# Optimization experiments

Measured on AMD Instinct MI355X. Metric: run time of the kernel, lower is better.

Reference implementation:

```python
import jax, jax.numpy as jnp
import numpy as np

BN_EPSILON = 1e-05


def hard_sigmoid(x):
    return jnp.clip((x + 1.0) / 2.0, 0.0, 1.0)


def setup_inputs() -> dict:
    key = jax.random.key(0)
    kx, kw, kb = jax.random.split(key, 3)
    # NHWC activations
    x = jax.random.normal(kx, (64, 112, 112, 64), dtype=jnp.float32)
    # HWIO kernel initialized ~ truncated_normal(stddev=0.2), then Bernoulli-binarized
    # to +/-1 once at graph-construction time (set_input_shape), so we sample here.
    k_init = 0.2 * jax.random.normal(kw, (3, 3, 64, 64), dtype=jnp.float32)
    kernels = 2.0 * jax.random.bernoulli(kb, hard_sigmoid(k_init)).astype(jnp.float32) - 1.0
    # tf.contrib.layers.batch_norm defaults: center=True (beta), scale=False (no gamma)
    beta = jnp.zeros((64,), dtype=jnp.float32)
    return {"x": x, "kernels": kernels, "beta": beta}


def reference(x, kernels, beta):
    # Training-mode batch norm: per-batch moments over (N, H, W)
    mean = jnp.mean(x, axis=(0, 1, 2))
    var = jnp.var(x, axis=(0, 1, 2))
    x_bn = (x - mean) * jax.lax.rsqrt(var + BN_EPSILON) + beta
    # NOTE: original code computes conv(sign(x_bn), k) but immediately overwrites it
    # with conv(x_bn, k); the effective forward uses the batch-normed (non-signed)
    # activations with the binarized (+/-1) kernels.
    a = jax.lax.conv_general_dilated(
        x_bn, kernels,
        window_strides=(1, 1),
        padding="SAME",
        dimension_numbers=("NHWC", "HWIO", "NHWC"),
    )
    return a
```

## Files before the change

kernel.cpp:

```cpp
#include <hip/hip_runtime.h>

typedef __attribute__((ext_vector_type(8))) short bf16x8;
typedef __attribute__((ext_vector_type(8))) unsigned short u16x8;
typedef __attribute__((ext_vector_type(4))) unsigned short u16x4;
typedef __attribute__((ext_vector_type(4))) float f32x4;

#define HW      112
#define CH      64
#define PIX_IMG (HW*HW)
#define N4TOT   (64*112*112*64/4)
#define NPIX_F  802816.0f

#define WS_HV_BYTE  1280
#define WS_W_BYTE   4096
#define WS_XBF_BYTE (4u<<20)

__device__ __forceinline__ unsigned short f2bf(float f) {
  unsigned u = __float_as_uint(f);
  u += 0x7FFFu + ((u >> 16) & 1u);
  return (unsigned short)(u >> 16);
}

__global__ void zero_ws(float* __restrict__ ws) {
  ws[threadIdx.x] = 0.0f;
}

template <bool WRITE_BF>
__global__ __launch_bounds__(256) void stats_kernel(const float* __restrict__ x,
                                                    float* __restrict__ ws,
                                                    unsigned short* __restrict__ xbf) {
  __shared__ float red[128];
  const int tid = threadIdx.x;
  if (tid < 128) red[tid] = 0.0f;
  __syncthreads();

  const f32x4* __restrict__ x4 = (const f32x4*)x;
  f32x4 s = {0.f, 0.f, 0.f, 0.f};
  f32x4 q = {0.f, 0.f, 0.f, 0.f};
  const int stride = gridDim.x * 256;
  #pragma unroll 4
  for (int i = blockIdx.x * 256 + tid; i < N4TOT; i += stride) {
    f32x4 v = __builtin_nontemporal_load(&x4[i]);
    s += v;
    q += v * v;
    if (WRITE_BF) {
      u16x4 o = {f2bf(v[0]), f2bf(v[1]), f2bf(v[2]), f2bf(v[3])};
      *(u16x4*)(xbf + 4 * i) = o;
    }
  }
  #pragma unroll
  for (int m = 16; m <= 32; m <<= 1) {
    #pragma unroll
    for (int j = 0; j < 4; ++j) {
      s[j] += __shfl_xor(s[j], m);
      q[j] += __shfl_xor(q[j], m);
    }
  }
  if ((tid & 63) < 16) {
    const int c0 = (tid & 15) * 4;
    #pragma unroll
    for (int j = 0; j < 4; ++j) {
      atomicAdd(&red[c0 + j], s[j]);
      atomicAdd(&red[64 + c0 + j], q[j]);
    }
  }
  __syncthreads();
  if (tid < 128) atomicAdd(&ws[tid], red[tid]);
}

__global__ __launch_bounds__(256) void finalize_kernel(const float* __restrict__ beta,
                                                       const float* __restrict__ k,
                                                       float* __restrict__ ws) {
  __shared__ float sb[64];
  __shared__ float part[256];
  const int tid = threadIdx.x;
  if (tid < 64) {
    float mean = ws[tid] * (1.0f / NPIX_F);
    float var  = fmaxf(ws[64 + tid] * (1.0f / NPIX_F) - mean * mean, 0.0f);
    float sc = rsqrtf(var + 1e-5f);
    float b  = beta[tid] - mean * sc;
    ws[128 + tid] = sc;
    ws[192 + tid] = b;
    ((unsigned short*)((char*)ws + WS_HV_BYTE))[tid] = f2bf(-b / sc);
    sb[tid] = b;
  }
  __syncthreads();
  const int co = tid & 63, pt = tid >> 6;
  float a = 0.f;
  #pragma unroll 8
  for (int t = pt; t < 576; t += 4)
    a = fmaf(sb[t & 63], k[t * 64 + co], a);
  part[tid] = a;
  __syncthreads();
  if (tid < 64)
    ws[256 + tid] = part[tid] + part[64 + tid] + part[128 + tid] + part[192 + tid];
}

__global__ __launch_bounds__(256) void prep_w(const float* __restrict__ k,
                                              const float* __restrict__ ws,
                                              unsigned short* __restrict__ wsw) {
  const int oidx = blockIdx.x * 256 + threadIdx.x;
  const int j  = oidx & 7;
  const int co = (oidx >> 3) & 63;
  const int qd = (oidx >> 9) & 3;
  const int t2 = oidx >> 11;
  const int tap = t2 % 9;
  const int h   = t2 / 9;
  const int ci  = h * 32 + qd * 8 + j;
  wsw[oidx] = f2bf(k[(tap * 64 + ci) * 64 + co] * ws[128 + ci]);
}

template <bool USE_BF>
__global__ __launch_bounds__(448, 4) void conv_kernel(const float* __restrict__ x,
                                                      const unsigned short* __restrict__ xbf,
                                                      const unsigned short* __restrict__ wsw,
                                                      const float* __restrict__ ws,
                                                      float* __restrict__ out) {
  __shared__ unsigned short Xs[4 * 6 * 114 * 8];
  __shared__ unsigned short Wd[2304 * 8];
  const int tid = threadIdx.x;
  int bid = (int)blockIdx.x;
  bid = (bid & 7) * 224 + (bid >> 3);
  const int n  = bid / 28;
  const int h0 = (bid % 28) * 4;

  const int lane = tid & 63;
  const int wv   = tid >> 6;
  const int qd   = lane >> 4;
  const int cc   = lane & 15;
  const int wvb  = wv * 16;

  const unsigned short* hv = (const unsigned short*)((const char*)ws + WS_HV_BYTE);

  f32x4 acc[4][4];
  {
    const float* bo = ws + 256;
    #pragma unroll
    for (int mt = 0; mt < 4; ++mt) {
      const f32x4 bv = *(const f32x4*)(bo + mt * 16 + qd * 4);
      #pragma unroll
      for (int r = 0; r < 4; ++r) acc[r][mt] = bv;
    }
  }

  for (int half = 0; half < 2; ++half) {
    {
      u16x8 hv8[4];
      #pragma unroll
      for (int o = 0; o < 4; ++o) hv8[o] = *(const u16x8*)(hv + half * 32 + o * 8);
      auto stage = [&](int c) {
        const int o  = c & 3;
        const int pi = c >> 2;
        const int p  = pi % 114;
        const int r  = pi / 114;
        const int w  = p - 1;
        const int g  = h0 + r - 1;
        u16x8 v;
        if ((unsigned)w < 112u && (unsigned)g < 112u) {
          const int base = ((n * 112 + g) * 112 + w) * 64 + half * 32 + o * 8;
          if (USE_BF) {
            v = *(const u16x8*)(xbf + base);
          } else {
            const float* sp = x + base;
            const f32x4 a = *(const f32x4*)sp;
            const f32x4 b = *(const f32x4*)(sp + 4);
            v = (u16x8){f2bf(a[0]), f2bf(a[1]), f2bf(a[2]), f2bf(a[3]),
                        f2bf(b[0]), f2bf(b[1]), f2bf(b[2]), f2bf(b[3])};
          }
        } else {
          v = hv8[o];
        }
        *(u16x8*)(&Xs[o * 5472 + pi * 8]) = v;
      };
      #pragma unroll
      for (int kk = 0; kk < 6; ++kk) stage(kk * 448 + tid);
      if (tid < 48) stage(2688 + tid);
    }
    {
      const unsigned short* wh = wsw + half * 18432;
      auto wstage = [&](int t) {
        *(u16x8*)(&Wd[t * 8]) = *(const u16x8*)(wh + t * 8);
      };
      #pragma unroll
      for (int kk = 0; kk < 5; ++kk) wstage(kk * 448 + tid);
      if (tid < 64) wstage(2240 + tid);
    }
    __syncthreads();

    #pragma unroll
    for (int dw = 0; dw < 3; ++dw) {
      bf16x8 xb[4];
      #pragma unroll
      for (int rr = 0; rr < 4; ++rr)
        xb[rr] = *(const bf16x8*)(&Xs[qd * 5472 + (rr * 114 + wvb + dw + cc) * 8]);
      #pragma unroll
      for (int dh = 0; dh < 3; ++dh) {
        if (dh)
          xb[(dh + 3) & 3] =
              *(const bf16x8*)(&Xs[qd * 5472 + ((dh + 3) * 114 + wvb + dw + cc) * 8]);
        #pragma unroll
        for (int mt = 0; mt < 4; ++mt) {
          const bf16x8 wa = *(const bf16x8*)(
              &Wd[(((dh * 3 + dw) * 4 + qd) * 64 + mt * 16 + cc) * 8]);
          #pragma unroll
          for (int r = 0; r < 4; ++r)
            acc[r][mt] = __builtin_amdgcn_mfma_f32_16x16x32_bf16(wa, xb[(dh + r) & 3],
                                                                 acc[r][mt], 0, 0, 0);
        }
      }
    }
    if (half == 0) __syncthreads();
  }

  #pragma unroll
  for (int r = 0; r < 4; ++r) {
    const int pix = n * PIX_IMG + (h0 + r) * 112 + wvb + cc;
    float* op = out + pix * 64 + qd * 4;
    #pragma unroll
    for (int mt = 0; mt < 4; ++mt)
      *(f32x4*)(op + mt * 16) = acc[r][mt];
  }
}

extern "C" void kernel_launch(void* const* d_in, const int* in_sizes, int n_in,
                              void* d_out, int out_size, void* d_ws, size_t ws_size,
                              hipStream_t stream) {
  const float* x    = (const float*)d_in[0];
  const float* kern = (const float*)d_in[1];
  const float* beta = (const float*)d_in[2];
  float* out = (float*)d_out;
  float* ws  = (float*)d_ws;
  unsigned short* wsw = (unsigned short*)((char*)d_ws + WS_W_BYTE);
  unsigned short* xbf = (unsigned short*)((char*)d_ws + WS_XBF_BYTE);

  const bool use_bf = ws_size >= (size_t)WS_XBF_BYTE + 102760448ull;

  zero_ws<<<1, 128, 0, stream>>>(ws);
  if (use_bf) stats_kernel<true ><<<2048, 256, 0, stream>>>(x, ws, xbf);
  else        stats_kernel<false><<<2048, 256, 0, stream>>>(x, ws, xbf);
  finalize_kernel<<<1, 256, 0, stream>>>(beta, kern, ws);
  prep_w<<<144, 256, 0, stream>>>(kern, ws, wsw);
  if (use_bf) conv_kernel<true ><<<64 * 28, 448, 0, stream>>>(x, xbf, wsw, ws, out);
  else        conv_kernel<false><<<64 * 28, 448, 0, stream>>>(x, xbf, wsw, ws, out);
}
```

Baseline: 493.3 us.

## Give each wave a private input tile, prefetch second channel half, fuse finalize/prep

The conv kernel now loads all weights for both channel halves into shared memory once. Each wave gets its own 6x18 halo tile, so the block-wide barriers between halves go away. Global loads for the second channel half go into registers before the first half's MFMA work and are written to the wave's tile afterwards, overlapping memory with compute. Finalize and weight-prep are merged into one launch, and the block-index swizzle is dropped. The trade is more LDS per block (launch bounds cut from 4 to 2 blocks per CU, so lower occupancy), more register pressure from the prefetch buffer, and redundant halo loads across neighbouring waves.

```diff
diff --git a/kernel.cpp b/kernel.cpp
--- a/kernel.cpp
+++ b/kernel.cpp
@@ -68,9 +68,11 @@
   if (tid < 128) atomicAdd(&ws[tid], red[tid]);
 }
 
-__global__ __launch_bounds__(256) void finalize_kernel(const float* __restrict__ beta,
-                                                       const float* __restrict__ k,
-                                                       float* __restrict__ ws) {
+__global__ __launch_bounds__(256) void finalize_prep(const float* __restrict__ beta,
+                                                     const float* __restrict__ k,
+                                                     float* __restrict__ ws,
+                                                     unsigned short* __restrict__ wsw) {
+  __shared__ float scl[64];
   __shared__ float sb[64];
   __shared__ float part[256];
   const int tid = threadIdx.x;
@@ -79,48 +81,48 @@
     float var  = fmaxf(ws[64 + tid] * (1.0f / NPIX_F) - mean * mean, 0.0f);
     float sc = rsqrtf(var + 1e-5f);
     float b  = beta[tid] - mean * sc;
-    ws[128 + tid] = sc;
-    ws[192 + tid] = b;
-    ((unsigned short*)((char*)ws + WS_HV_BYTE))[tid] = f2bf(-b / sc);
-    sb[tid] = b;
-  }
-  __syncthreads();
-  const int co = tid & 63, pt = tid >> 6;
-  float a = 0.f;
-  #pragma unroll 8
-  for (int t = pt; t < 576; t += 4)
-    a = fmaf(sb[t & 63], k[t * 64 + co], a);
-  part[tid] = a;
-  __syncthreads();
-  if (tid < 64)
-    ws[256 + tid] = part[tid] + part[64 + tid] + part[128 + tid] + part[192 + tid];
-}
-
-__global__ __launch_bounds__(256) void prep_w(const float* __restrict__ k,
-                                              const float* __restrict__ ws,
-                                              unsigned short* __restrict__ wsw) {
-  const int oidx = blockIdx.x * 256 + threadIdx.x;
-  const int j  = oidx & 7;
-  const int co = (oidx >> 3) & 63;
-  const int qd = (oidx >> 9) & 3;
-  const int t2 = oidx >> 11;
-  const int tap = t2 % 9;
-  const int h   = t2 / 9;
-  const int ci  = h * 32 + qd * 8 + j;
-  wsw[oidx] = f2bf(k[(tap * 64 + ci) * 64 + co] * ws[128 + ci]);
+    scl[tid] = sc;
+    sb[tid]  = b;
+    if (blockIdx.x == 0)
+      ((unsigned short*)((char*)ws + WS_HV_BYTE))[tid] = f2bf(-b / sc);
+  }
+  __syncthreads();
+
+  {
+    const int oidx = blockIdx.x * 256 + tid;
+    const int j  = oidx & 7;
+    const int co = (oidx >> 3) & 63;
+    const int qd = (oidx >> 9) & 3;
+    const int t2 = oidx >> 11;
+    const int tap = t2 % 9;
+    const int h   = t2 / 9;
+    const int ci  = h * 32 + qd * 8 + j;
+    wsw[oidx] = f2bf(k[(tap * 64 + ci) * 64 + co] * scl[ci]);
+  }
+
+  if (blockIdx.x == 0) {
+    const int co = tid & 63, pt = tid >> 6;
+    float a = 0.f;
+    #pragma unroll 8
+    for (int t = pt; t < 576; t += 4)
+      a = fmaf(sb[t & 63], k[t * 64 + co], a);
+    part[tid] = a;
+    __syncthreads();
+    if (tid < 64)
+      ws[256 + tid] = part[tid] + part[64 + tid] + part[128 + tid] + part[192 + tid];
+  }
 }
 
 template <bool USE_BF>
-__global__ __launch_bounds__(448, 4) void conv_kernel(const float* __restrict__ x,
+__global__ __launch_bounds__(448, 2) void conv_kernel(const float* __restrict__ x,
                                                       const unsigned short* __restrict__ xbf,
                                                       const unsigned short* __restrict__ wsw,
                                                       const float* __restrict__ ws,
                                                       float* __restrict__ out) {
-  __shared__ unsigned short Xs[4 * 6 * 114 * 8];
-  __shared__ unsigned short Wd[2304 * 8];
+  __shared__ unsigned short Xs[7 * 3456];
+  __shared__ unsigned short Wd[36864];
   const int tid = threadIdx.x;
-  int bid = (int)blockIdx.x;
-  bid = (bid & 7) * 224 + (bid >> 3);
+  const int bid = (int)blockIdx.x;
   const int n  = bid / 28;
   const int h0 = (bid % 28) * 4;
 
@@ -131,6 +133,7 @@
   const int wvb  = wv * 16;
 
   const unsigned short* hv = (const unsigned short*)((const char*)ws + WS_HV_BYTE);
+  unsigned short* Xw = &Xs[wv * 3456];
 
   f32x4 acc[4][4];
   {
@@ -143,21 +146,25 @@
     }
   }
 
-  for (int half = 0; half < 2; ++half) {
-    {
-      u16x8 hv8[4];
-      #pragma unroll
-      for (int o = 0; o < 4; ++o) hv8[o] = *(const u16x8*)(hv + half * 32 + o * 8);
-      auto stage = [&](int c) {
-        const int o  = c & 3;
-        const int pi = c >> 2;
-        const int p  = pi % 114;
-        const int r  = pi / 114;
-        const int w  = p - 1;
-        const int g  = h0 + r - 1;
+  for (int t = tid; t < 4608; t += 448)
+    *(u16x8*)(&Wd[t * 8]) = *(const u16x8*)(wsw + t * 8);
+  __syncthreads();
+
+
+  {
+    u16x8 hv8[4];
+    #pragma unroll
+    for (int o = 0; o < 4; ++o) hv8[o] = *(const u16x8*)(hv + o * 8);
+    #pragma unroll
+    for (int kk = 0; kk < 7; ++kk) {
+      const int e = kk * 64 + lane;
+      if (kk < 6 || lane < 48) {
+        const int o = e & 3, r2 = e >> 2;
+        const int px = r2 % 18, row = r2 / 18;
+        const int w = wvb + px - 1, g = h0 + row - 1;
         u16x8 v;
         if ((unsigned)w < 112u && (unsigned)g < 112u) {
-          const int base = ((n * 112 + g) * 112 + w) * 64 + half * 32 + o * 8;
+          const int base = ((n * 112 + g) * 112 + w) * 64 + o * 8;
           if (USE_BF) {
             v = *(const u16x8*)(xbf + base);
           } else {
@@ -170,38 +177,44 @@
         } else {
           v = hv8[o];
         }
-        *(u16x8*)(&Xs[o * 5472 + pi * 8]) = v;
-      };
-      #pragma unroll
-      for (int kk = 0; kk < 6; ++kk) stage(kk * 448 + tid);
-      if (tid < 48) stage(2688 + tid);
-    }
-    {
-      const unsigned short* wh = wsw + half * 18432;
-      auto wstage = [&](int t) {
-        *(u16x8*)(&Wd[t * 8]) = *(const u16x8*)(wh + t * 8);
-      };
-      #pragma unroll
-      for (int kk = 0; kk < 5; ++kk) wstage(kk * 448 + tid);
-      if (tid < 64) wstage(2240 + tid);
-    }
-    __syncthreads();
-
+        *(u16x8*)(&Xw[o * 864 + r2 * 8]) = v;
+      }
+    }
+  }
+
+  u16x8 pf[7];
+  if (USE_BF) {
+    #pragma unroll
+    for (int kk = 0; kk < 7; ++kk) {
+      const int e = kk * 64 + lane;
+      if (kk < 6 || lane < 48) {
+        const int o = e & 3, r2 = e >> 2;
+        const int px = r2 % 18, row = r2 / 18;
+        const int w = wvb + px - 1, g = h0 + row - 1;
+        if ((unsigned)w < 112u && (unsigned)g < 112u)
+          pf[kk] = *(const u16x8*)(xbf + ((n * 112 + g) * 112 + w) * 64 + 32 + o * 8);
+      }
+    }
+    __builtin_amdgcn_sched_barrier(0);
+  }
+
+  auto compute = [&](int half) {
+    const int wb = half * 18432;
     #pragma unroll
     for (int dw = 0; dw < 3; ++dw) {
       bf16x8 xb[4];
       #pragma unroll
       for (int rr = 0; rr < 4; ++rr)
-        xb[rr] = *(const bf16x8*)(&Xs[qd * 5472 + (rr * 114 + wvb + dw + cc) * 8]);
+        xb[rr] = *(const bf16x8*)(&Xw[qd * 864 + (rr * 18 + dw + cc) * 8]);
       #pragma unroll
       for (int dh = 0; dh < 3; ++dh) {
         if (dh)
           xb[(dh + 3) & 3] =
-              *(const bf16x8*)(&Xs[qd * 5472 + ((dh + 3) * 114 + wvb + dw + cc) * 8]);
+              *(const bf16x8*)(&Xw[qd * 864 + ((dh + 3) * 18 + dw + cc) * 8]);
         #pragma unroll
         for (int mt = 0; mt < 4; ++mt) {
           const bf16x8 wa = *(const bf16x8*)(
-              &Wd[(((dh * 3 + dw) * 4 + qd) * 64 + mt * 16 + cc) * 8]);
+              &Wd[wb + (((dh * 3 + dw) * 4 + qd) * 64 + mt * 16 + cc) * 8]);
           #pragma unroll
           for (int r = 0; r < 4; ++r)
             acc[r][mt] = __builtin_amdgcn_mfma_f32_16x16x32_bf16(wa, xb[(dh + r) & 3],
@@ -209,8 +222,42 @@
         }
       }
     }
-    if (half == 0) __syncthreads();
-  }
+  };
+
+  compute(0);
+
+  {
+    u16x8 hv8[4];
+    #pragma unroll
+    for (int o = 0; o < 4; ++o) hv8[o] = *(const u16x8*)(hv + 32 + o * 8);
+    #pragma unroll
+    for (int kk = 0; kk < 7; ++kk) {
+      const int e = kk * 64 + lane;
+      if (kk < 6 || lane < 48) {
+        const int o = e & 3, r2 = e >> 2;
+        const int px = r2 % 18, row = r2 / 18;
+        const int w = wvb + px - 1, g = h0 + row - 1;
+        const bool ok = (unsigned)w < 112u && (unsigned)g < 112u;
+        u16x8 v;
+        if (USE_BF) {
+          v = ok ? pf[kk] : hv8[o];
+        } else {
+          if (ok) {
+            const float* sp = x + ((n * 112 + g) * 112 + w) * 64 + 32 + o * 8;
+            const f32x4 a = *(const f32x4*)sp;
+            const f32x4 b = *(const f32x4*)(sp + 4);
+            v = (u16x8){f2bf(a[0]), f2bf(a[1]), f2bf(a[2]), f2bf(a[3]),
+                        f2bf(b[0]), f2bf(b[1]), f2bf(b[2]), f2bf(b[3])};
+          } else {
+            v = hv8[o];
+          }
+        }
+        *(u16x8*)(&Xw[o * 864 + r2 * 8]) = v;
+      }
+    }
+  }
+
+  compute(1);
 
   #pragma unroll
   for (int r = 0; r < 4; ++r) {
@@ -238,8 +285,7 @@
   zero_ws<<<1, 128, 0, stream>>>(ws);
   if (use_bf) stats_kernel<true ><<<2048, 256, 0, stream>>>(x, ws, xbf);
   else        stats_kernel<false><<<2048, 256, 0, stream>>>(x, ws, xbf);
-  finalize_kernel<<<1, 256, 0, stream>>>(beta, kern, ws);
-  prep_w<<<144, 256, 0, stream>>>(kern, ws, wsw);
+  finalize_prep<<<144, 256, 0, stream>>>(beta, kern, ws, wsw);
   if (use_bf) conv_kernel<true ><<<64 * 28, 448, 0, stream>>>(x, xbf, wsw, ws, out);
   else        conv_kernel<false><<<64 * 28, 448, 0, stream>>>(x, xbf, wsw, ws, out);
 }
```

Measured after the change: 517.6 us. +4.9%, slower.

## Use per-wave LDS input tiles, split row staging, fuse finalize with weight prep

Applied to the files above, without the earlier changes.

The conv kernel now stages a private 6-row by 18-pixel input strip per wave instead of one shared tile for the whole block. The first four rows are computed before the last two are loaded, so waves no longer wait on each other for input data and LDS use drops. The blockIdx swizzle is removed. The separate finalize and prep_w kernels are merged into one 144-block launch, removing a launch and a dependency, at the cost of every block recomputing the BN scale. The per-wave halo pixels are loaded redundantly, and dropping the swizzle may change L2 locality.

```diff
diff --git a/kernel.cpp b/kernel.cpp
--- a/kernel.cpp
+++ b/kernel.cpp
@@ -68,9 +68,11 @@
   if (tid < 128) atomicAdd(&ws[tid], red[tid]);
 }
 
-__global__ __launch_bounds__(256) void finalize_kernel(const float* __restrict__ beta,
-                                                       const float* __restrict__ k,
-                                                       float* __restrict__ ws) {
+__global__ __launch_bounds__(256) void finalize_prep(const float* __restrict__ beta,
+                                                     const float* __restrict__ k,
+                                                     float* __restrict__ ws,
+                                                     unsigned short* __restrict__ wsw) {
+  __shared__ float scl[64];
   __shared__ float sb[64];
   __shared__ float part[256];
   const int tid = threadIdx.x;
@@ -79,35 +81,36 @@
     float var  = fmaxf(ws[64 + tid] * (1.0f / NPIX_F) - mean * mean, 0.0f);
     float sc = rsqrtf(var + 1e-5f);
     float b  = beta[tid] - mean * sc;
-    ws[128 + tid] = sc;
-    ws[192 + tid] = b;
-    ((unsigned short*)((char*)ws + WS_HV_BYTE))[tid] = f2bf(-b / sc);
-    sb[tid] = b;
-  }
-  __syncthreads();
-  const int co = tid & 63, pt = tid >> 6;
-  float a = 0.f;
-  #pragma unroll 8
-  for (int t = pt; t < 576; t += 4)
-    a = fmaf(sb[t & 63], k[t * 64 + co], a);
-  part[tid] = a;
-  __syncthreads();
-  if (tid < 64)
-    ws[256 + tid] = part[tid] + part[64 + tid] + part[128 + tid] + part[192 + tid];
-}
-
-__global__ __launch_bounds__(256) void prep_w(const float* __restrict__ k,
-                                              const float* __restrict__ ws,
-                                              unsigned short* __restrict__ wsw) {
-  const int oidx = blockIdx.x * 256 + threadIdx.x;
-  const int j  = oidx & 7;
-  const int co = (oidx >> 3) & 63;
-  const int qd = (oidx >> 9) & 3;
-  const int t2 = oidx >> 11;
-  const int tap = t2 % 9;
-  const int h   = t2 / 9;
-  const int ci  = h * 32 + qd * 8 + j;
-  wsw[oidx] = f2bf(k[(tap * 64 + ci) * 64 + co] * ws[128 + ci]);
+    scl[tid] = sc;
+    sb[tid]  = b;
+    if (blockIdx.x == 0)
+      ((unsigned short*)((char*)ws + WS_HV_BYTE))[tid] = f2bf(-b / sc);
+  }
+  __syncthreads();
+
+  {
+    const int oidx = blockIdx.x * 256 + tid;
+    const int j  = oidx & 7;
+    const int co = (oidx >> 3) & 63;
+    const int qd = (oidx >> 9) & 3;
+    const int t2 = oidx >> 11;
+    const int tap = t2 % 9;
+    const int h   = t2 / 9;
+    const int ci  = h * 32 + qd * 8 + j;
+    wsw[oidx] = f2bf(k[(tap * 64 + ci) * 64 + co] * scl[ci]);
+  }
+
+  if (blockIdx.x == 0) {
+    const int co = tid & 63, pt = tid >> 6;
+    float a = 0.f;
+    #pragma unroll 8
+    for (int t = pt; t < 576; t += 4)
+      a = fmaf(sb[t & 63], k[t * 64 + co], a);
+    part[tid] = a;
+    __syncthreads();
+    if (tid < 64)
+      ws[256 + tid] = part[tid] + part[64 + tid] + part[128 + tid] + part[192 + tid];
+  }
 }
 
 template <bool USE_BF>
@@ -116,11 +119,10 @@
                                                       const unsigned short* __restrict__ wsw,
                                                       const float* __restrict__ ws,
                                                       float* __restrict__ out) {
-  __shared__ unsigned short Xs[4 * 6 * 114 * 8];
-  __shared__ unsigned short Wd[2304 * 8];
+  __shared__ unsigned short Xs[7 * 2304];
+  __shared__ unsigned short Wd[18432];
   const int tid = threadIdx.x;
-  int bid = (int)blockIdx.x;
-  bid = (bid & 7) * 224 + (bid >> 3);
+  const int bid = (int)blockIdx.x;
   const int n  = bid / 28;
   const int h0 = (bid % 28) * 4;
 
@@ -131,6 +133,7 @@
   const int wvb  = wv * 16;
 
   const unsigned short* hv = (const unsigned short*)((const char*)ws + WS_HV_BYTE);
+  unsigned short* Xw = &Xs[wv * 2304];
 
   f32x4 acc[4][4];
   {
@@ -143,74 +146,112 @@
     }
   }
 
-  for (int half = 0; half < 2; ++half) {
-    {
-      u16x8 hv8[4];
-      #pragma unroll
-      for (int o = 0; o < 4; ++o) hv8[o] = *(const u16x8*)(hv + half * 32 + o * 8);
-      auto stage = [&](int c) {
-        const int o  = c & 3;
-        const int pi = c >> 2;
-        const int p  = pi % 114;
-        const int r  = pi / 114;
-        const int w  = p - 1;
-        const int g  = h0 + r - 1;
-        u16x8 v;
-        if ((unsigned)w < 112u && (unsigned)g < 112u) {
-          const int base = ((n * 112 + g) * 112 + w) * 64 + half * 32 + o * 8;
-          if (USE_BF) {
-            v = *(const u16x8*)(xbf + base);
-          } else {
-            const float* sp = x + base;
-            const f32x4 a = *(const f32x4*)sp;
-            const f32x4 b = *(const f32x4*)(sp + 4);
-            v = (u16x8){f2bf(a[0]), f2bf(a[1]), f2bf(a[2]), f2bf(a[3]),
-                        f2bf(b[0]), f2bf(b[1]), f2bf(b[2]), f2bf(b[3])};
-          }
-        } else {
-          v = hv8[o];
-        }
-        *(u16x8*)(&Xs[o * 5472 + pi * 8]) = v;
-      };
-      #pragma unroll
-      for (int kk = 0; kk < 6; ++kk) stage(kk * 448 + tid);
-      if (tid < 48) stage(2688 + tid);
-    }
-    {
-      const unsigned short* wh = wsw + half * 18432;
-      auto wstage = [&](int t) {
-        *(u16x8*)(&Wd[t * 8]) = *(const u16x8*)(wh + t * 8);
-      };
-      #pragma unroll
-      for (int kk = 0; kk < 5; ++kk) wstage(kk * 448 + tid);
-      if (tid < 64) wstage(2240 + tid);
-    }
-    __syncthreads();
-
+  auto ld = [&](int g, int w, int q, int half, const u16x8 hv8[4]) -> u16x8 {
+    if ((unsigned)w < 112u && (unsigned)g < 112u) {
+      const int base = ((n * 112 + g) * 112 + w) * 64 + half * 32 + q * 8;
+      if (USE_BF) {
+        return *(const u16x8*)(xbf + base);
+      } else {
+        const float* sp = x + base;
+        const f32x4 a = *(const f32x4*)sp;
+        const f32x4 b = *(const f32x4*)(sp + 4);
+        return (u16x8){f2bf(a[0]), f2bf(a[1]), f2bf(a[2]), f2bf(a[3]),
+                       f2bf(b[0]), f2bf(b[1]), f2bf(b[2]), f2bf(b[3])};
+      }
+    }
+    return hv8[q];
+  };
+
+  auto stageA = [&](int half) {
+    u16x8 hv8[4];
+    #pragma unroll
+    for (int o = 0; o < 4; ++o) hv8[o] = *(const u16x8*)(hv + half * 32 + o * 8);
+    #pragma unroll
+    for (int kk = 0; kk < 5; ++kk) {
+      const int c = kk * 64 + lane;
+      if (kk < 4 || lane < 32) {
+        const int q = c & 3, r2 = c >> 2;
+        const int s = r2 / 18, px = r2 % 18;
+        const u16x8 v = ld(h0 + s - 1, wvb + px - 1, q, half, hv8);
+        *(u16x8*)(&Xw[s * 576 + q * 144 + px * 8]) = v;
+      }
+    }
+  };
+
+  auto stageB = [&](int half) {
+    u16x8 hv8[4];
+    #pragma unroll
+    for (int o = 0; o < 4; ++o) hv8[o] = *(const u16x8*)(hv + half * 32 + o * 8);
+    #pragma unroll
+    for (int kk = 0; kk < 3; ++kk) {
+      const int c = kk * 64 + lane;
+      if (kk < 2 || lane < 16) {
+        const int q = c & 3, r2 = c >> 2;
+        const int s = r2 / 18, px = r2 % 18;
+        const u16x8 v = ld(h0 + 3 + s, wvb + px - 1, q, half, hv8);
+        *(u16x8*)(&Xw[s * 576 + q * 144 + px * 8]) = v;
+      }
+    }
+  };
+
+  auto computeA = [&]() {
     #pragma unroll
     for (int dw = 0; dw < 3; ++dw) {
       bf16x8 xb[4];
       #pragma unroll
-      for (int rr = 0; rr < 4; ++rr)
-        xb[rr] = *(const bf16x8*)(&Xs[qd * 5472 + (rr * 114 + wvb + dw + cc) * 8]);
+      for (int s = 0; s < 4; ++s)
+        xb[s] = *(const bf16x8*)(&Xw[s * 576 + qd * 144 + (dw + cc) * 8]);
       #pragma unroll
       for (int dh = 0; dh < 3; ++dh) {
-        if (dh)
-          xb[(dh + 3) & 3] =
-              *(const bf16x8*)(&Xs[qd * 5472 + ((dh + 3) * 114 + wvb + dw + cc) * 8]);
         #pragma unroll
         for (int mt = 0; mt < 4; ++mt) {
           const bf16x8 wa = *(const bf16x8*)(
               &Wd[(((dh * 3 + dw) * 4 + qd) * 64 + mt * 16 + cc) * 8]);
           #pragma unroll
-          for (int r = 0; r < 4; ++r)
-            acc[r][mt] = __builtin_amdgcn_mfma_f32_16x16x32_bf16(wa, xb[(dh + r) & 3],
-                                                                 acc[r][mt], 0, 0, 0);
+          for (int o = 0; o < 4 - dh; ++o)
+            acc[o][mt] = __builtin_amdgcn_mfma_f32_16x16x32_bf16(wa, xb[o + dh],
+                                                                 acc[o][mt], 0, 0, 0);
         }
       }
     }
-    if (half == 0) __syncthreads();
-  }
+  };
+
+  auto computeB = [&]() {
+    #pragma unroll
+    for (int dw = 0; dw < 3; ++dw) {
+      const bf16x8 x4 = *(const bf16x8*)(&Xw[0 * 576 + qd * 144 + (dw + cc) * 8]);
+      const bf16x8 x5 = *(const bf16x8*)(&Xw[1 * 576 + qd * 144 + (dw + cc) * 8]);
+      #pragma unroll
+      for (int dh = 1; dh < 3; ++dh) {
+        #pragma unroll
+        for (int mt = 0; mt < 4; ++mt) {
+          const bf16x8 wa = *(const bf16x8*)(
+              &Wd[(((dh * 3 + dw) * 4 + qd) * 64 + mt * 16 + cc) * 8]);
+          #pragma unroll
+          for (int o = 4 - dh; o < 4; ++o)
+            acc[o][mt] = __builtin_amdgcn_mfma_f32_16x16x32_bf16(
+                wa, (o + dh == 4) ? x4 : x5, acc[o][mt], 0, 0, 0);
+        }
+      }
+    }
+  };
+
+  for (int t = tid; t < 2304; t += 448)
+    *(u16x8*)(&Wd[t * 8]) = *(const u16x8*)(wsw + t * 8);
+  stageA(0);
+  __syncthreads();
+  computeA();
+  stageB(0);
+  computeB();
+
+  stageA(1);
+  __syncthreads();
+  for (int t = tid; t < 2304; t += 448)
+    *(u16x8*)(&Wd[t * 8]) = *(const u16x8*)(wsw + 18432 + t * 8);
+  __syncthreads();
+  computeA();
+  stageB(1);
+  computeB();
 
   #pragma unroll
   for (int r = 0; r < 4; ++r) {
@@ -238,8 +279,7 @@
   zero_ws<<<1, 128, 0, stream>>>(ws);
   if (use_bf) stats_kernel<true ><<<2048, 256, 0, stream>>>(x, ws, xbf);
   else        stats_kernel<false><<<2048, 256, 0, stream>>>(x, ws, xbf);
-  finalize_kernel<<<1, 256, 0, stream>>>(beta, kern, ws);
-  prep_w<<<144, 256, 0, stream>>>(kern, ws, wsw);
+  finalize_prep<<<144, 256, 0, stream>>>(beta, kern, ws, wsw);
   if (use_bf) conv_kernel<true ><<<64 * 28, 448, 0, stream>>>(x, xbf, wsw, ws, out);
   else        conv_kernel<false><<<64 * 28, 448, 0, stream>>>(x, xbf, wsw, ws, out);
 }
```

Measured after the change: 551.2 us. +11.7%, slower.
